# Performance work log

Hardware: AMD Instinct MI355X
Metric: run time of the kernel (lower is better)

Reference implementation:

```python
import jax, jax.numpy as jnp
import numpy as np

EPS = 1e-8
TINY = 1e-12
C_L1 = float(np.sqrt(3.0 / (4.0 * np.pi)))  # integral-normalized l=1 SH coefficient


def _elu_feature_map(x):
    # positive_feature_map(kind='elu'): elu(x) + 1 > 0
    return jax.nn.elu(x) + 1.0


def _sph_bessel_j1(x):
    # j1(x) = sin(x)/x^2 - cos(x)/x, with series x/3 near 0 for stability
    small = x < 1e-4
    xs = jnp.where(small, 1.0, x)
    return jnp.where(small, x / 3.0, jnp.sin(xs) / (xs * xs) - jnp.cos(xs) / xs)


def setup_inputs() -> dict:
    key = jax.random.key(0)
    k1, k2, k3, k4, k5 = jax.random.split(key, 5)
    B, N, H, D, C, Q = 1, 2048, 8, 32, 32, 8
    pos = jax.random.normal(k1, (B, N, 3), dtype=jnp.float32) * 5.0
    q = jax.random.normal(k2, (B, N, H, D), dtype=jnp.float32)
    k = jax.random.normal(k3, (B, N, H, D), dtype=jnp.float32)
    v = jax.random.normal(k4, (B, N, H, C), dtype=jnp.float32)
    kappa = jnp.linspace(0.5, 4.0, Q, dtype=jnp.float32)          # (Q,) buffer
    a = jax.random.normal(k5, (H, Q), dtype=jnp.float32) * 0.1    # (H,Q) -> 'head' mode
    node_mask = jnp.ones((B, N), dtype=bool)
    return {"pos": pos, "q": q, "k": k, "v": v, "kappa": kappa, "a": a, "node_mask": node_mask}


def reference(pos, q, k, v, kappa, a, node_mask):
    B, N = pos.shape[0], pos.shape[1]
    m = node_mask.astype(pos.dtype)  # (B,N)

    # Linear (kernel) attention: alpha[b,h,i,j] = <phi(q_i), phi(k_j)> / sum_n <phi(q_i), phi(k_n)>
    phi_q = _elu_feature_map(q) * m[:, :, None, None]
    phi_k = _elu_feature_map(k) * m[:, :, None, None]
    v_m = v * m[:, :, None, None]
    logits = jnp.einsum('bihd,bjhd->bhij', phi_q, phi_k)
    denom = jnp.maximum(logits.sum(axis=-1, keepdims=True), EPS)
    alpha = logits / denom  # (B,H,N,N)

    # Pairwise geometry
    r_ij = pos[:, :, None, :] - pos[:, None, :, :]            # (B,N,N,3)
    dist = jnp.sqrt(jnp.sum(r_ij * r_ij, axis=-1) + TINY)     # (B,N,N)
    eye = jnp.eye(N, dtype=bool)
    safe_vec = jnp.array([1.0, 0.0, 0.0], dtype=pos.dtype)
    r_safe = jnp.where(eye[None, :, :, None], safe_vec, r_ij)

    # Real spherical harmonics, l=1, integral normalization, on normalized r_ij
    rn = jnp.sqrt(jnp.sum(r_safe * r_safe, axis=-1, keepdims=True) + TINY)
    Y = C_L1 * (r_safe / rn)  # (B,N,N,3) -> M=3 components

    # Radial part: f[b,h,i,j] = sum_q a[h,q] * j1(dist_ij * kappa_q)
    x = dist[..., None] * kappa  # (B,N,N,Q)
    jl = _sph_bessel_j1(x)
    f = jnp.einsum('bijq,hq->bhij', jl, a)

    # out[b,i,h,m,c] = sum_j alpha*f * Y * v
    w = alpha * f
    out = jnp.einsum('bhij,bijm,bjhc->bihmc', w, Y, v_m)
    return out  # (B, N, H, 2l+1=3, C)
```

## Files before the change

### kernel.cpp

```cpp
#include <hip/hip_runtime.h>

#define NN   2048
#define NH   8
#define ND   32
#define NC   32
#define NQ   8
#define JS   8
#define NOUT (NN*NH*3*NC)
#define EPSV 1e-8f
#define TINYV 1e-12f
#define C_L1 0.4886025119029199f

typedef _Float16 half8 __attribute__((ext_vector_type(8)));
typedef __fp16   fp16x2 __attribute__((ext_vector_type(2)));
typedef float    f32x4 __attribute__((ext_vector_type(4)));

__device__ __forceinline__ float phi_elu(float x) { return x > 0.f ? x + 1.f : __expf(x); }
__device__ __forceinline__ float rfl(float x) {
    return __int_as_float(__builtin_amdgcn_readfirstlane(__float_as_int(x)));
}
__device__ __forceinline__ void glds16(const void* g, void* l) {
    __builtin_amdgcn_global_load_lds(
        (const __attribute__((address_space(1))) void*)g,
        (__attribute__((address_space(3))) void*)l, 16, 0, 0);
}

__global__ void k_prep(const float* __restrict__ pos, const float* __restrict__ q,
                       const float* __restrict__ k, const float* __restrict__ v,
                       const float* __restrict__ a,
                       _Float16* __restrict__ phiQ16, _Float16* __restrict__ KtF,
                       _Float16* __restrict__ VtF, float* __restrict__ posT,
                       float* __restrict__ ksum, float* __restrict__ coef) {
    int b = blockIdx.x, t = threadIdx.x;
    if (b < 256) {
        int h = t >> 5, d = t & 31;
        int dg = d >> 3, e = d & 7;
        float ks = 0.f;
        for (int jj = 0; jj < 8; ++jj) {
            int j = b * 8 + jj;
            float pq = phi_elu(q[j * 256 + t]);
            float pk = phi_elu(k[j * 256 + t]);
            phiQ16[j * 256 + t] = (_Float16)pq;
            int jblk = j >> 5, jin = j & 31, jf = jin >> 4, lo = jin & 15;
            KtF[((((h * 64 + jblk) * 2 + jf) * 64) + dg * 16 + lo) * 8 + e] = (_Float16)pk;
            ks += pk;
        }
        atomicAdd(&ksum[t], ks);
    } else if (b < 512) {
        int unit = (b - 256) * 4 + (t >> 6);
        int lane = t & 63;
        int h = unit >> 7, jblk = (unit >> 1) & 63, cf = unit & 1;
        int hgrp = h >> 2, hh = h & 3;
        int c = cf * 16 + (lane & 15);
        int g8 = lane >> 4;
        half8 w0, w1, w2, w3;
        #pragma unroll
        for (int e = 0; e < 8; ++e) {
            int jl = g8 * 4 + (e & 3) + 16 * (e >> 2);
            int j = jblk * 32 + jl;
            float vv = v[(j * NH + h) * NC + c];
            w0[e] = (_Float16)vv;
            w1[e] = (_Float16)(vv * pos[j * 3 + 0]);
            w2[e] = (_Float16)(vv * pos[j * 3 + 1]);
            w3[e] = (_Float16)(vv * pos[j * 3 + 2]);
        }
        size_t fb = ((size_t)(jblk * 2 + hgrp) * 32 + hh * 2 + cf) * 64 + lane;
        ((half8*)VtF)[fb]        = w0;
        ((half8*)VtF)[fb + 512]  = w1;
        ((half8*)VtF)[fb + 1024] = w2;
        ((half8*)VtF)[fb + 1536] = w3;
    } else if (b < 536) {
        int idx = (b - 512) * 256 + t;
        if (idx < 3 * NN) {
            int comp = idx >> 11, j = idx & 2047;
            posT[comp * NN + j] = pos[j * 3 + comp];
        }
    } else {
        if (t < NH) {
            float An[8];
            #pragma unroll
            for (int n = 0; n < 8; ++n) An[n] = a[t * NQ + n];
            const float Tc[9][9] = {
                {0,0,0,0,0,0,0,0,0},
                {0,1,0,0,0,0,0,0,0},
                {-1,0,2,0,0,0,0,0,0},
                {0,-3,0,4,0,0,0,0,0},
                {1,0,-8,0,8,0,0,0,0},
                {0,5,0,-20,0,16,0,0,0},
                {-1,0,18,0,-48,0,32,0,0},
                {0,-7,0,56,0,-112,0,64,0},
                {1,0,-32,0,160,0,-256,0,128}};
            const float Uc[9][8] = {
                {0,0,0,0,0,0,0,0},
                {1,0,0,0,0,0,0,0},
                {0,2,0,0,0,0,0,0},
                {-1,0,4,0,0,0,0,0},
                {0,-4,0,8,0,0,0,0},
                {1,0,-12,0,16,0,0,0},
                {0,6,0,-32,0,32,0,0},
                {-1,0,24,0,-80,0,64,0},
                {0,-8,0,80,0,-192,0,128}};
            #pragma unroll
            for (int kk = 0; kk < 9; ++kk) {
                float s = 0.f;
                #pragma unroll
                for (int n = 1; n <= 8; ++n) s = fmaf(An[n-1] * (1.f / n), Tc[n][kk], s);
                coef[kk * 8 + t] = s;
            }
            #pragma unroll
            for (int kk = 0; kk < 8; ++kk) {
                float s = 0.f;
                #pragma unroll
                for (int n = 1; n <= 8; ++n) s = fmaf(An[n-1] * (1.f / (n * n)), Uc[n][kk], s);
                coef[(9 + kk) * 8 + t] = s;
            }
        }
    }
}

__global__ void k_dinv(const _Float16* __restrict__ phiQ16, const float* __restrict__ ksum,
                       float* __restrict__ dinv) {
    int g = blockIdx.x * 256 + threadIdx.x;
    int h = g & 7;
    const half8* qv = (const half8*)phiQ16 + (size_t)g * 4;
    float s = 0.f;
    #pragma unroll
    for (int d4 = 0; d4 < 4; ++d4) {
        half8 x = qv[d4];
        #pragma unroll
        for (int e = 0; e < 8; ++e) s += (float)x[e] * ksum[h * 32 + d4 * 8 + e];
    }
    dinv[g] = C_L1 / fmaxf(s, EPSV);
}

__global__ __launch_bounds__(256, 2)
void k_main(const float* __restrict__ posT, const _Float16* __restrict__ phiQ16,
            const _Float16* __restrict__ KtF, const _Float16* __restrict__ VtF,
            const float* __restrict__ kappa, const float* __restrict__ coef,
            const float* __restrict__ dinvb, float* __restrict__ part,
            float* __restrict__ out) {
    __shared__ __align__(16) char smem[2 * 32768];
    int tid = threadIdx.x;
    int wid = tid >> 6, lane = tid & 63;
    int li = lane & 15, g = lane >> 4;

    int bid = blockIdx.x;
    int hgrp = bid & 1, js = (bid >> 1) & 7, ib = bid >> 4;
    int itile = ib * 64 + wid * 16;

    float k0  = rfl(kappa[0]);
    float ik0 = rfl(1.f / kappa[0]);

    float pc[4][9], qc[4][8];
    #pragma unroll
    for (int hh = 0; hh < 4; ++hh) {
        #pragma unroll
        for (int kk = 0; kk < 9; ++kk) pc[hh][kk] = rfl(coef[kk * 8 + hgrp * 4 + hh]);
        #pragma unroll
        for (int kk = 0; kk < 8; ++kk) qc[hh][kk] = rfl(coef[(9 + kk) * 8 + hgrp * 4 + hh]);
    }

    half8 qa[4];
    #pragma unroll
    for (int hh = 0; hh < 4; ++hh)
        qa[hh] = ((const half8*)phiQ16)[((size_t)(itile + li) * NH + hgrp * 4 + hh) * 4 + g];

    float pi0 = posT[itile + li];
    float pi1 = posT[NN + itile + li];
    float pi2 = posT[2 * NN + itile + li];

    f32x4 acc[4][4][2];
    #pragma unroll
    for (int hh = 0; hh < 4; ++hh)
      #pragma unroll
      for (int pl = 0; pl < 4; ++pl)
        #pragma unroll
        for (int cf = 0; cf < 2; ++cf)
          acc[hh][pl][cf] = (f32x4){0.f, 0.f, 0.f, 0.f};

    const int j0 = js * (NN / JS);
    const int NCHUNK = (NN / JS) / 32;
    const f32x4 z4 = (f32x4){0.f, 0.f, 0.f, 0.f};

    {
        int jb2 = ((j0 >> 5) * 2 + hgrp);
        const char* src = (const char*)VtF + ((size_t)jb2 << 15) + wid * 8192 + lane * 16;
        char* dstl = smem + wid * 8192 + lane * 16;
        #pragma unroll
        for (int kk = 0; kk < 8; ++kk)
            glds16(src + kk * 1024, dstl + kk * 1024);
    }

    #pragma unroll 1
    for (int t = 0; t < NCHUNK; ++t) {
        int jc = j0 + t * 32, jblk = jc >> 5;

        f32x4 pj4[3][2];
        #pragma unroll
        for (int m = 0; m < 3; ++m)
            #pragma unroll
            for (int jF = 0; jF < 2; ++jF)
                pj4[m][jF] = *(const f32x4*)(posT + m * NN + jc + jF * 16 + g * 4);

        union { half8 h; fp16x2 p[4]; } wa[4];

        #pragma unroll
        for (int jF = 0; jF < 2; ++jF) {
            f32x4 s[4];
            #pragma unroll
            for (int hh = 0; hh < 4; ++hh) {
                int h = hgrp * 4 + hh;
                half8 kf = ((const half8*)KtF)[((h * 64 + jblk) * 2 + jF) * 64 + lane];
                s[hh] = __builtin_amdgcn_mfma_f32_16x16x32_f16(kf, qa[hh], z4, 0, 0, 0);
            }

            float gux[4][4];
            #pragma unroll
            for (int r = 0; r < 4; ++r) {
                float dx = pi0 - pj4[0][jF][r];
                float dy = pi1 - pj4[1][jF][r];
                float dz = pi2 - pj4[2][jF][r];
                float d2 = fmaf(dx, dx, fmaf(dy, dy, fmaf(dz, dz, TINYV)));
                float u = rsqrtf(d2);
                u = (d2 < 1e-10f) ? 0.f : u;
                float dist = d2 * u;
                float th = dist * k0;
                float sth, cth;
                __sincosf(th, &sth, &cth);
                float e1 = u * u * ik0;
                float ws = u * ik0 * sth;
                #pragma unroll
                for (int hh = 0; hh < 4; ++hh) {
                    float P = pc[hh][8];
                    #pragma unroll
                    for (int kk = 7; kk >= 0; --kk) P = fmaf(P, cth, pc[hh][kk]);
                    float Qv = qc[hh][7];
                    #pragma unroll
                    for (int kk = 6; kk >= 0; --kk) Qv = fmaf(Qv, cth, qc[hh][kk]);
                    float inner = fmaf(ws, Qv, -P);
                    gux[hh][r] = s[hh][r] * (e1 * inner);
                }
            }
            #pragma unroll
            for (int hh = 0; hh < 4; ++hh) {
                wa[hh].p[jF * 2 + 0] = __builtin_amdgcn_cvt_pkrtz(gux[hh][0], gux[hh][1]);
                wa[hh].p[jF * 2 + 1] = __builtin_amdgcn_cvt_pkrtz(gux[hh][2], gux[hh][3]);
            }
        }

        __syncthreads();

        const char* vb = smem + (t & 1) * 32768;
        #pragma unroll
        for (int hh = 0; hh < 4; ++hh) {
            #pragma unroll
            for (int pl = 0; pl < 4; ++pl) {
                half8 vf0 = *(const half8*)(vb + ((pl * 4 + hh) * 2 + 0) * 1024 + lane * 16);
                half8 vf1 = *(const half8*)(vb + ((pl * 4 + hh) * 2 + 1) * 1024 + lane * 16);
                acc[hh][pl][0] = __builtin_amdgcn_mfma_f32_16x16x32_f16(wa[hh].h, vf0, acc[hh][pl][0], 0, 0, 0);
                acc[hh][pl][1] = __builtin_amdgcn_mfma_f32_16x16x32_f16(wa[hh].h, vf1, acc[hh][pl][1], 0, 0, 0);
            }
        }

        if (t + 1 < NCHUNK) {
            int jb2 = ((jblk + 1) * 2 + hgrp);
            const char* src = (const char*)VtF + ((size_t)jb2 << 15) + wid * 8192 + lane * 16;
            char* dstl = smem + ((t + 1) & 1) * 32768 + wid * 8192 + lane * 16;
            #pragma unroll
            for (int kk = 0; kk < 8; ++kk)
                glds16(src + kk * 1024, dstl + kk * 1024);
        }
    }

    f32x4 pi_ep[3];
    #pragma unroll
    for (int m = 0; m < 3; ++m)
        pi_ep[m] = *(const f32x4*)(posT + m * NN + itile + g * 4);

    float* dst = (js == JS - 1) ? out : part + (size_t)js * NOUT;
    #pragma unroll
    for (int hh = 0; hh < 4; ++hh) {
        int h = hgrp * 4 + hh;
        float dv[4];
        #pragma unroll
        for (int r = 0; r < 4; ++r) dv[r] = dinvb[(itile + g * 4 + r) * NH + h];
        #pragma unroll
        for (int m = 0; m < 3; ++m)
        #pragma unroll
        for (int cf = 0; cf < 2; ++cf)
        #pragma unroll
        for (int r = 0; r < 4; ++r) {
            int i = itile + g * 4 + r;
            float val = fmaf(pi_ep[m][r], acc[hh][0][cf][r], -acc[hh][m + 1][cf][r]);
            dst[((size_t)i * NH + h) * 96 + m * 32 + cf * 16 + li] = val * dv[r];
        }
    }
}

__global__ void k_reduce(const float4* __restrict__ part, float4* __restrict__ out) {
    int e = blockIdx.x * 256 + threadIdx.x;
    const int NOUT4 = NOUT / 4;
    if (e >= NOUT4) return;
    float4 s = out[e];
    #pragma unroll
    for (int p = 0; p < JS - 1; ++p) {
        float4 t = part[(size_t)p * NOUT4 + e];
        s.x += t.x; s.y += t.y; s.z += t.z; s.w += t.w;
    }
    out[e] = s;
}

extern "C" void kernel_launch(void* const* d_in, const int* in_sizes, int n_in,
                              void* d_out, int out_size, void* d_ws, size_t ws_size,
                              hipStream_t stream) {
    const float* pos   = (const float*)d_in[0];
    const float* q     = (const float*)d_in[1];
    const float* k     = (const float*)d_in[2];
    const float* v     = (const float*)d_in[3];
    const float* kappa = (const float*)d_in[4];
    const float* a     = (const float*)d_in[5];
    float* out = (float*)d_out;
    char* ws = (char*)d_ws;

    _Float16* phiQ16 = (_Float16*)(ws + 0);
    _Float16* KtF    = (_Float16*)(ws + (1u << 20));
    _Float16* VtF    = (_Float16*)(ws + (2u << 20));
    float*    posT   = (float*)   (ws + (6u << 20));
    float*    ksum   = (float*)   (ws + (6u << 20) + 24576);
    float*    dinvb  = (float*)   (ws + (6u << 20) + 25600);
    float*    coefb  = (float*)   (ws + (6u << 20) + 91136);
    float*    partb  = (float*)   (ws + (6u << 20) + 131072);

    (void)hipMemsetAsync(ksum, 0, 256 * sizeof(float), stream);
    k_prep<<<537, 256, 0, stream>>>(pos, q, k, v, a, phiQ16, KtF, VtF, posT, ksum, coefb);
    k_dinv<<<NN * NH / 256, 256, 0, stream>>>(phiQ16, ksum, dinvb);
    k_main<<<(NN / 64) * 2 * JS, 256, 0, stream>>>(posT, phiQ16, KtF, VtF,
                                                   kappa, coefb, dinvb, partb, out);
    k_reduce<<<(NOUT / 4 + 255) / 256, 256, 0, stream>>>((const float4*)partb, (float4*)out);
}
```

Baseline: 72.34 us.

## Store split-J partials in scaled fp16 and pack radial polynomial evaluation

The split-J partial sums are now written as fp16, scaled by 128, and the reduce kernel reads half8 vectors and rescales them. This halves the partial-buffer traffic in both k_main and k_reduce. The 1/kappa factors are also folded into the precomputed Chebyshev coefficients, and the P and Q Horner chains are evaluated together as paired f32x2 FMAs to cut VALU work in the inner loop. The fp16 partials lose precision and could overflow or underflow for outputs outside the scaled range.

Result: faster. 69.30 us (-4.2%).

```diff
diff --git a/kernel.cpp b/kernel.cpp
--- a/kernel.cpp
+++ b/kernel.cpp
@@ -10,10 +10,12 @@
 #define EPSV 1e-8f
 #define TINYV 1e-12f
 #define C_L1 0.4886025119029199f
+#define PSCALE 128.0f
 
 typedef _Float16 half8 __attribute__((ext_vector_type(8)));
 typedef __fp16   fp16x2 __attribute__((ext_vector_type(2)));
 typedef float    f32x4 __attribute__((ext_vector_type(4)));
+typedef float    f32x2 __attribute__((ext_vector_type(2)));
 
 __device__ __forceinline__ float phi_elu(float x) { return x > 0.f ? x + 1.f : __expf(x); }
 __device__ __forceinline__ float rfl(float x) {
@@ -27,7 +29,7 @@
 
 __global__ void k_prep(const float* __restrict__ pos, const float* __restrict__ q,
                        const float* __restrict__ k, const float* __restrict__ v,
-                       const float* __restrict__ a,
+                       const float* __restrict__ kappa, const float* __restrict__ a,
                        _Float16* __restrict__ phiQ16, _Float16* __restrict__ KtF,
                        _Float16* __restrict__ VtF, float* __restrict__ posT,
                        float* __restrict__ ksum, float* __restrict__ coef) {
@@ -80,6 +82,8 @@
             float An[8];
             #pragma unroll
             for (int n = 0; n < 8; ++n) An[n] = a[t * NQ + n];
+            float k0 = kappa[0];
+            float ik0 = 1.f / k0, ik02 = ik0 * ik0;
             const float Tc[9][9] = {
                 {0,0,0,0,0,0,0,0,0},
                 {0,1,0,0,0,0,0,0,0},
@@ -105,14 +109,14 @@
                 float s = 0.f;
                 #pragma unroll
                 for (int n = 1; n <= 8; ++n) s = fmaf(An[n-1] * (1.f / n), Tc[n][kk], s);
-                coef[kk * 8 + t] = s;
+                coef[kk * 8 + t] = s * ik0;
             }
             #pragma unroll
             for (int kk = 0; kk < 8; ++kk) {
                 float s = 0.f;
                 #pragma unroll
                 for (int n = 1; n <= 8; ++n) s = fmaf(An[n-1] * (1.f / (n * n)), Uc[n][kk], s);
-                coef[(9 + kk) * 8 + t] = s;
+                coef[(9 + kk) * 8 + t] = s * ik02;
             }
         }
     }
@@ -137,7 +141,7 @@
 void k_main(const float* __restrict__ posT, const _Float16* __restrict__ phiQ16,
             const _Float16* __restrict__ KtF, const _Float16* __restrict__ VtF,
             const float* __restrict__ kappa, const float* __restrict__ coef,
-            const float* __restrict__ dinvb, float* __restrict__ part,
+            const float* __restrict__ dinvb, _Float16* __restrict__ part,
             float* __restrict__ out) {
     __shared__ __align__(16) char smem[2 * 32768];
     int tid = threadIdx.x;
@@ -148,16 +152,21 @@
     int hgrp = bid & 1, js = (bid >> 1) & 7, ib = bid >> 4;
     int itile = ib * 64 + wid * 16;
 
-    float k0  = rfl(kappa[0]);
-    float ik0 = rfl(1.f / kappa[0]);
-
-    float pc[4][9], qc[4][8];
+    float k0 = rfl(kappa[0]);
+
+    float pc0[4];
+    f32x2 cpq[4][8];
     #pragma unroll
     for (int hh = 0; hh < 4; ++hh) {
-        #pragma unroll
-        for (int kk = 0; kk < 9; ++kk) pc[hh][kk] = rfl(coef[kk * 8 + hgrp * 4 + hh]);
-        #pragma unroll
-        for (int kk = 0; kk < 8; ++kk) qc[hh][kk] = rfl(coef[(9 + kk) * 8 + hgrp * 4 + hh]);
+        int h = hgrp * 4 + hh;
+        pc0[hh] = rfl(coef[h]);
+        cpq[hh][0][0] = rfl(coef[8 * 8 + h]);
+        cpq[hh][0][1] = rfl(coef[(9 + 7) * 8 + h]);
+        #pragma unroll
+        for (int kk = 1; kk <= 7; ++kk) {
+            cpq[hh][kk][0] = rfl(coef[kk * 8 + h]);
+            cpq[hh][kk][1] = rfl(coef[(9 + kk - 1) * 8 + h]);
+        }
     }
 
     half8 qa[4];
@@ -227,18 +236,18 @@
                 float th = dist * k0;
                 float sth, cth;
                 __sincosf(th, &sth, &cth);
-                float e1 = u * u * ik0;
-                float ws = u * ik0 * sth;
+                float e1 = u * u;
+                float ws = u * sth;
+                f32x2 cc; cc[0] = cth; cc[1] = cth;
                 #pragma unroll
                 for (int hh = 0; hh < 4; ++hh) {
-                    float P = pc[hh][8];
+                    f32x2 pq = cpq[hh][0];
                     #pragma unroll
-                    for (int kk = 7; kk >= 0; --kk) P = fmaf(P, cth, pc[hh][kk]);
-                    float Qv = qc[hh][7];
-                    #pragma unroll
-                    for (int kk = 6; kk >= 0; --kk) Qv = fmaf(Qv, cth, qc[hh][kk]);
-                    float inner = fmaf(ws, Qv, -P);
-                    gux[hh][r] = s[hh][r] * (e1 * inner);
+                    for (int kk = 7; kk >= 1; --kk)
+                        pq = __builtin_elementwise_fma(pq, cc, cpq[hh][kk]);
+                    float P = fmaf(pq[0], cth, pc0[hh]);
+                    float inner = fmaf(ws, pq[1], -P);
+                    gux[hh][r] = (s[hh][r] * e1) * inner;
                 }
             }
             #pragma unroll
@@ -277,13 +286,17 @@
     for (int m = 0; m < 3; ++m)
         pi_ep[m] = *(const f32x4*)(posT + m * NN + itile + g * 4);
 
-    float* dst = (js == JS - 1) ? out : part + (size_t)js * NOUT;
+    bool last = (js == JS - 1);
+    _Float16* pdst = part + (size_t)js * NOUT;
     #pragma unroll
     for (int hh = 0; hh < 4; ++hh) {
         int h = hgrp * 4 + hh;
         float dv[4];
         #pragma unroll
-        for (int r = 0; r < 4; ++r) dv[r] = dinvb[(itile + g * 4 + r) * NH + h];
+        for (int r = 0; r < 4; ++r) {
+            dv[r] = dinvb[(itile + g * 4 + r) * NH + h];
+            if (!last) dv[r] *= PSCALE;
+        }
         #pragma unroll
         for (int m = 0; m < 3; ++m)
         #pragma unroll
@@ -291,23 +304,34 @@
         #pragma unroll
         for (int r = 0; r < 4; ++r) {
             int i = itile + g * 4 + r;
-            float val = fmaf(pi_ep[m][r], acc[hh][0][cf][r], -acc[hh][m + 1][cf][r]);
-            dst[((size_t)i * NH + h) * 96 + m * 32 + cf * 16 + li] = val * dv[r];
-        }
-    }
-}
-
-__global__ void k_reduce(const float4* __restrict__ part, float4* __restrict__ out) {
+            size_t idx = ((size_t)i * NH + h) * 96 + m * 32 + cf * 16 + li;
+            float val = fmaf(pi_ep[m][r], acc[hh][0][cf][r], -acc[hh][m + 1][cf][r]) * dv[r];
+            if (last) out[idx] = val;
+            else      pdst[idx] = (_Float16)val;
+        }
+    }
+}
+
+__global__ void k_reduce(const _Float16* __restrict__ part, float4* __restrict__ out) {
     int e = blockIdx.x * 256 + threadIdx.x;
-    const int NOUT4 = NOUT / 4;
-    if (e >= NOUT4) return;
-    float4 s = out[e];
+    const int NO8 = NOUT / 8;
+    if (e >= NO8) return;
+    float4 o0 = out[e * 2], o1 = out[e * 2 + 1];
+    const float S = 1.f / PSCALE;
     #pragma unroll
     for (int p = 0; p < JS - 1; ++p) {
-        float4 t = part[(size_t)p * NOUT4 + e];
-        s.x += t.x; s.y += t.y; s.z += t.z; s.w += t.w;
-    }
-    out[e] = s;
+        half8 t = ((const half8*)part)[(size_t)p * NO8 + e];
+        o0.x = fmaf((float)t[0], S, o0.x);
+        o0.y = fmaf((float)t[1], S, o0.y);
+        o0.z = fmaf((float)t[2], S, o0.z);
+        o0.w = fmaf((float)t[3], S, o0.w);
+        o1.x = fmaf((float)t[4], S, o1.x);
+        o1.y = fmaf((float)t[5], S, o1.y);
+        o1.z = fmaf((float)t[6], S, o1.z);
+        o1.w = fmaf((float)t[7], S, o1.w);
+    }
+    out[e * 2] = o0;
+    out[e * 2 + 1] = o1;
 }
 
 extern "C" void kernel_launch(void* const* d_in, const int* in_sizes, int n_in,
@@ -329,12 +353,13 @@
     float*    ksum   = (float*)   (ws + (6u << 20) + 24576);
     float*    dinvb  = (float*)   (ws + (6u << 20) + 25600);
     float*    coefb  = (float*)   (ws + (6u << 20) + 91136);
-    float*    partb  = (float*)   (ws + (6u << 20) + 131072);
+    _Float16* partb  = (_Float16*)(ws + (6u << 20) + 131072);
 
     (void)hipMemsetAsync(ksum, 0, 256 * sizeof(float), stream);
-    k_prep<<<537, 256, 0, stream>>>(pos, q, k, v, a, phiQ16, KtF, VtF, posT, ksum, coefb);
+    k_prep<<<537, 256, 0, stream>>>(pos, q, k, v, kappa, a,
+                                    phiQ16, KtF, VtF, posT, ksum, coefb);
     k_dinv<<<NN * NH / 256, 256, 0, stream>>>(phiQ16, ksum, dinvb);
     k_main<<<(NN / 64) * 2 * JS, 256, 0, stream>>>(posT, phiQ16, KtF, VtF,
                                                    kappa, coefb, dinvb, partb, out);
-    k_reduce<<<(NOUT / 4 + 255) / 256, 256, 0, stream>>>((const float4*)partb, (float4*)out);
-}
+    k_reduce<<<(NOUT / 8 + 255) / 256, 256, 0, stream>>>(partb, (float4*)out);
+}
```
